# Performance work log

Hardware: AMD Instinct MI355X
Metric: run time of the kernel (lower is better)

Reference implementation:

```python
import jax, jax.numpy as jnp
import numpy as np

NUM_GRAPHS = 1024
NODES = 1024          # nodes per graph (ring length)
N = NUM_GRAPHS * NODES
H = 64


def setup_inputs() -> dict:
    key = jax.random.key(0)
    ks = jax.random.split(key, 4)
    node_index = jax.random.normal(ks[0], (N, 3), dtype=jnp.float32)
    # per-graph ring edges (intended behavior of the torch code)
    i = jnp.arange(N, dtype=jnp.int64)
    g = i // NODES
    src = i
    dst = g * NODES + (i + 1) % NODES
    edge_index = jnp.stack([src, dst])  # [2, N]
    # glorot-ish weights, zero biases (PyG GCNConv default bias=True)
    W1 = jax.random.normal(ks[1], (3, H), dtype=jnp.float32) * (1.0 / np.sqrt(3.0))
    b1 = jnp.zeros((H,), dtype=jnp.float32)
    W2 = jax.random.normal(ks[2], (H, H), dtype=jnp.float32) * (1.0 / np.sqrt(H))
    b2 = jnp.zeros((H,), dtype=jnp.float32)
    Wl = jax.random.normal(ks[3], (H, 3), dtype=jnp.float32) * (1.0 / np.sqrt(H))
    bl = jnp.zeros((3,), dtype=jnp.float32)
    return {"node_index": node_index, "edge_index": edge_index,
            "W1": W1, "b1": b1, "W2": W2, "b2": b2, "Wl": Wl, "bl": bl}


def gcn_layer(x, W, b, src, dst):
    """PyG GCNConv: symmetric-normalized aggregation with self-loops.
    out[j] = sum_{i->j} (deg_i * deg_j)^-0.5 * (x_i @ W) + b
    """
    n = x.shape[0]
    h = x @ W                                   # [n, out]
    loop = jnp.arange(n, dtype=src.dtype)
    s = jnp.concatenate([src, loop])
    d = jnp.concatenate([dst, loop])
    deg = jax.ops.segment_sum(jnp.ones(d.shape[0], dtype=h.dtype), d, num_segments=n)
    dinv = jnp.where(deg > 0, jax.lax.rsqrt(jnp.maximum(deg, 1e-12)), 0.0)
    norm = dinv[s] * dinv[d]                    # [E+n]
    msg = h[s] * norm[:, None]                  # gather + scale
    out = jax.ops.segment_sum(msg, d, num_segments=n)  # scatter-add
    return out + b


def reference(node_index, edge_index, W1, b1, W2, b2, Wl, bl):
    src, dst = edge_index[0], edge_index[1]
    x = jax.nn.relu(gcn_layer(node_index, W1, b1, src, dst))
    x = jax.nn.relu(gcn_layer(x, W2, b2, src, dst))
    return x @ Wl + bl
```

## Files before the change

kernel.cpp:

```cpp
#include <hip/hip_runtime.h>

#define NPG 1024
#define NT 256

typedef _Float16 half8 __attribute__((ext_vector_type(8)));
typedef _Float16 half4v __attribute__((ext_vector_type(4)));
typedef __fp16 fp16x2 __attribute__((ext_vector_type(2)));
typedef float floatx4 __attribute__((ext_vector_type(4)));
typedef unsigned int uint4v __attribute__((ext_vector_type(4)));

#define WS_W2F 0
#define WS_W1F 4096
#define WS_WLF 5120

__device__ __forceinline__ unsigned short f2h(float f) {
    union { _Float16 h; unsigned short u; } v; v.h = (_Float16)f; return v.u;
}
__device__ __forceinline__ float h2f(unsigned short u) {
    union { unsigned short u; _Float16 h; } v; v.u = u; return (float)v.h;
}
__device__ __forceinline__ unsigned int pack_h2(float a, float b) {
    union { fp16x2 h; unsigned int u; } v;
    v.h = __builtin_amdgcn_cvt_pkrtz(a, b);
    return v.u;
}
__device__ __forceinline__ int kperm(int k) {
    return ((k & 3)) | (((k >> 2) & 3) << 4) | (((k >> 4) & 3) << 2);
}

union Frag  { half8 h;  unsigned int u[4]; };
union Frag4 { half4v h; unsigned int u[2]; };
union Pack4 { uint4v u; half8 h; };

__global__ void gnn_prep(const float* __restrict__ W1,
                         const float* __restrict__ b1,
                         const float* __restrict__ W2,
                         const float* __restrict__ Wl,
                         unsigned short* __restrict__ ws)
{
    int idx = blockIdx.x * NT + threadIdx.x;
    if (idx >= 6144) return;
    float v;
    if (idx < 4096) {
        int l = (idx >> 3) & 63, j = idx & 7;
        int c16l = l & 15, quadl = l >> 4;
        int f = idx >> 9, ct = f >> 1, kb = f & 1;
        int o  = ct * 16 + c16l;
        int k  = kperm(kb * 32 + quadl * 8 + j);
        v = 0.5f * W2[k * 64 + o];
    } else if (idx < 5120) {
        int r = idx - 4096;
        int ct = r >> 8, rem = r & 255;
        int l = rem >> 2, j = rem & 3;
        int c16l = l & 15, quadl = l >> 4;
        v = 0.0f;
        if (quadl == 0)
            v = (j < 3) ? W1[j * 64 + ct * 16 + c16l] : b1[ct * 16 + c16l];
    } else {
        int r = idx - 5120;
        int l = (r >> 3) & 63, j = r & 7;
        int c16l = l & 15, quadl = l >> 4;
        int kb = r >> 9;
        int o = (2 * kb + (j >> 2)) * 16 + quadl * 4 + (j & 3);
        v = (c16l < 3) ? Wl[o * 3 + c16l] : 0.0f;
    }
    ws[idx] = f2h(v);
}

__global__ __launch_bounds__(NT, 4)
void gnn_main(const float* __restrict__ x0,
              const float* __restrict__ b2,
              const float* __restrict__ bl,
              const unsigned short* __restrict__ ws,
              float* __restrict__ out)
{
    __shared__ unsigned short sX1[2][65 * 72];
    __shared__ uint2 ySv[513];

    const int t    = threadIdx.x;
    const int lane = t & 63;
    const int w    = t >> 6;
    const int c16  = lane & 15;
    const int quad = lane >> 4;

    const int g     = blockIdx.x >> 1;
    const int base  = (blockIdx.x & 1) * 512;
    const int gbase = g * NPG;

    #pragma unroll
    for (int rr = 0; rr < 2; rr++) {
        int rl = t + rr * 256;
        int n1 = (base - 1 + rl) & (NPG - 1);
        int n0 = (n1 - 1) & (NPG - 1);
        const float* a = x0 + (gbase + n0) * 3;
        const float* b = x0 + (gbase + n1) * 3;
        uint2 pv;
        pv.x = pack_h2(0.5f * (a[0] + b[0]), 0.5f * (a[1] + b[1]));
        pv.y = pack_h2(0.5f * (a[2] + b[2]), 1.0f);
        ySv[rl] = pv;
    }
    if (t == 0) {
        int n1 = (base + 511) & (NPG - 1);
        int n0 = (n1 - 1) & (NPG - 1);
        const float* a = x0 + (gbase + n0) * 3;
        const float* b = x0 + (gbase + n1) * 3;
        uint2 pv;
        pv.x = pack_h2(0.5f * (a[0] + b[0]), 0.5f * (a[1] + b[1]));
        pv.y = pack_h2(0.5f * (a[2] + b[2]), 1.0f);
        ySv[512] = pv;
    }

    Frag4 w1f[4];
    #pragma unroll
    for (int ct = 0; ct < 4; ct++)
        w1f[ct].h = *(const half4v*)(ws + WS_W1F + ct * 256 + lane * 4);
    Frag a2[4][2];
    #pragma unroll
    for (int ct = 0; ct < 4; ct++)
        #pragma unroll
        for (int kb = 0; kb < 2; kb++)
            a2[ct][kb].h = *(const half8*)(ws + WS_W2F + (ct * 2 + kb) * 512 + lane * 8);
    Frag a3[2];
    #pragma unroll
    for (int kb = 0; kb < 2; kb++)
        a3[kb].h = *(const half8*)(ws + WS_WLF + kb * 512 + lane * 8);
    floatx4 b2v[4];
    #pragma unroll
    for (int ct = 0; ct < 4; ct++)
        b2v[ct] = *(const floatx4*)(b2 + ct * 16 + quad * 4);
    const float blv = (c16 < 3) ? bl[c16] : 0.0f;
    float w1c0 = 0.0f, w1c1 = 0.0f, w1c2 = 0.0f, w1b = 0.0f;
    if (t < 64) {
        const unsigned short* w1r = ws + WS_W1F + (t >> 4) * 256 + (t & 15) * 4;
        w1c0 = h2f(w1r[0]); w1c1 = h2f(w1r[1]); w1c2 = h2f(w1r[2]); w1b = h2f(w1r[3]);
    }

    __syncthreads();

    auto layer1 = [&](int p0, unsigned short* X1) {
        const int q = 16 * w + c16;
        Frag4 bfr1;
        bfr1.u[0] = bfr1.u[1] = 0;
        if (quad == 0) {
            uint2 pv = ySv[(p0 - base) + q];
            bfr1.u[0] = pv.x;
            bfr1.u[1] = pv.y;
        }
        floatx4 acc1[4];
        #pragma unroll
        for (int ct = 0; ct < 4; ct++) {
            floatx4 z = {0.0f, 0.0f, 0.0f, 0.0f};
            acc1[ct] = __builtin_amdgcn_mfma_f32_16x16x16f16(w1f[ct].h, bfr1.h, z, 0, 0, 0);
        }
        #pragma unroll
        for (int p = 0; p < 2; p++) {
            Pack4 dv;
            dv.u.x = pack_h2(acc1[2*p  ][0], acc1[2*p  ][1]);
            dv.u.y = pack_h2(acc1[2*p  ][2], acc1[2*p  ][3]);
            dv.u.z = pack_h2(acc1[2*p+1][0], acc1[2*p+1][1]);
            dv.u.w = pack_h2(acc1[2*p+1][2], acc1[2*p+1][3]);
            half8 z8 = {};
            dv.h = __builtin_elementwise_max(dv.h, z8);
            *(uint4v*)&X1[q * 72 + quad * 16 + p * 8] = dv.u;
        }
        if (t < 64) {
            uint2 pv = ySv[(p0 - base) + 64];
            float acc = w1b;
            acc = fmaf(h2f((unsigned short)(pv.x & 0xffff)), w1c0, acc);
            acc = fmaf(h2f((unsigned short)(pv.x >> 16)),    w1c1, acc);
            acc = fmaf(h2f((unsigned short)(pv.y & 0xffff)), w1c2, acc);
            X1[64 * 72 + kperm(t)] = f2h(fmaxf(acc, 0.0f));
        }
    };

    auto layer23 = [&](int p0, const unsigned short* X1) {
        const int q = 16 * w + c16;
        half8 bsum[2];
        #pragma unroll
        for (int kb = 0; kb < 2; kb++) {
            half8 r0 = *(const half8*)(&X1[(q    ) * 72 + kb * 32 + quad * 8]);
            half8 r1 = *(const half8*)(&X1[(q + 1) * 72 + kb * 32 + quad * 8]);
            bsum[kb] = r0 + r1;
        }
        floatx4 acc2[4];
        #pragma unroll
        for (int ct = 0; ct < 4; ct++) {
            floatx4 z = b2v[ct];
            z = __builtin_amdgcn_mfma_f32_16x16x32_f16(a2[ct][0].h, bsum[0], z, 0, 0, 0);
            z = __builtin_amdgcn_mfma_f32_16x16x32_f16(a2[ct][1].h, bsum[1], z, 0, 0, 0);
            acc2[ct] = z;
        }
        Frag pa[2];
        #pragma unroll
        for (int ct = 0; ct < 4; ct++) {
            pa[ct >> 1].u[(ct & 1) * 2    ] = pack_h2(acc2[ct][0], acc2[ct][1]);
            pa[ct >> 1].u[(ct & 1) * 2 + 1] = pack_h2(acc2[ct][2], acc2[ct][3]);
        }
        half8 z8 = {};
        pa[0].h = __builtin_elementwise_max(pa[0].h, z8);
        pa[1].h = __builtin_elementwise_max(pa[1].h, z8);
        floatx4 acc3 = {0.0f, 0.0f, 0.0f, 0.0f};
        acc3 = __builtin_amdgcn_mfma_f32_16x16x32_f16(pa[0].h, a3[0].h, acc3, 0, 0, 0);
        acc3 = __builtin_amdgcn_mfma_f32_16x16x32_f16(pa[1].h, a3[1].h, acc3, 0, 0, 0);
        if (c16 < 3) {
            float* po = out + (gbase + p0 + 16 * w + quad * 4) * 3 + c16;
            po[0] = acc3[0] + blv;
            po[3] = acc3[1] + blv;
            po[6] = acc3[2] + blv;
            po[9] = acc3[3] + blv;
        }
    };

    layer1(base, sX1[0]);
    __syncthreads();
    #pragma unroll
    for (int tl = 0; tl < 7; tl++) {
        layer1(base + (tl + 1) * 64, sX1[(tl + 1) & 1]);
        layer23(base + tl * 64, sX1[tl & 1]);
        __syncthreads();
    }
    layer23(base + 7 * 64, sX1[1]);
}

extern "C" void kernel_launch(void* const* d_in, const int* in_sizes, int n_in,
                              void* d_out, int out_size, void* d_ws, size_t ws_size,
                              hipStream_t stream) {
    const float* x0 = (const float*)d_in[0];
    const float* W1 = (const float*)d_in[2];
    const float* b1 = (const float*)d_in[3];
    const float* W2 = (const float*)d_in[4];
    const float* b2 = (const float*)d_in[5];
    const float* Wl = (const float*)d_in[6];
    const float* bl = (const float*)d_in[7];
    unsigned short* ws = (unsigned short*)d_ws;
    float* out = (float*)d_out;

    gnn_prep<<<24, NT, 0, stream>>>(W1, b1, W2, Wl, ws);
    gnn_main<<<2048, NT, 0, stream>>>(x0, b2, bl, ws, out);
}
```

Before: 98.17 us.

## Process one whole graph per block instead of half a graph

Each block now handles all 1024 nodes of a graph, so the grid is halved to 1024 blocks and the per-block prologue (weight fragment loads, bias loads) is amortized over twice the work. The smoothed-input staging buffer is doubled, and the tile loop is restructured as a non-unrolled loop with two tiles per iteration to keep code size in check. The cost is fewer blocks (1024 over 256 CUs) and more LDS per block, which may lower occupancy and leave tail imbalance.

```diff
diff --git a/kernel.cpp b/kernel.cpp
--- a/kernel.cpp
+++ b/kernel.cpp
@@ -75,7 +75,7 @@
               float* __restrict__ out)
 {
     __shared__ unsigned short sX1[2][65 * 72];
-    __shared__ uint2 ySv[513];
+    __shared__ uint2 ySv[1025];
 
     const int t    = threadIdx.x;
     const int lane = t & 63;
@@ -83,15 +83,14 @@
     const int c16  = lane & 15;
     const int quad = lane >> 4;
 
-    const int g     = blockIdx.x >> 1;
-    const int base  = (blockIdx.x & 1) * 512;
+    const int g     = blockIdx.x;
     const int gbase = g * NPG;
 
     #pragma unroll
-    for (int rr = 0; rr < 2; rr++) {
+    for (int rr = 0; rr < 4; rr++) {
         int rl = t + rr * 256;
-        int n1 = (base - 1 + rl) & (NPG - 1);
-        int n0 = (n1 - 1) & (NPG - 1);
+        int n1 = (rl - 1) & (NPG - 1);
+        int n0 = (rl - 2) & (NPG - 1);
         const float* a = x0 + (gbase + n0) * 3;
         const float* b = x0 + (gbase + n1) * 3;
         uint2 pv;
@@ -100,14 +99,12 @@
         ySv[rl] = pv;
     }
     if (t == 0) {
-        int n1 = (base + 511) & (NPG - 1);
-        int n0 = (n1 - 1) & (NPG - 1);
-        const float* a = x0 + (gbase + n0) * 3;
-        const float* b = x0 + (gbase + n1) * 3;
+        const float* a = x0 + (gbase + 1022) * 3;
+        const float* b = x0 + (gbase + 1023) * 3;
         uint2 pv;
         pv.x = pack_h2(0.5f * (a[0] + b[0]), 0.5f * (a[1] + b[1]));
         pv.y = pack_h2(0.5f * (a[2] + b[2]), 1.0f);
-        ySv[512] = pv;
+        ySv[1024] = pv;
     }
 
     Frag4 w1f[4];
@@ -142,7 +139,7 @@
         Frag4 bfr1;
         bfr1.u[0] = bfr1.u[1] = 0;
         if (quad == 0) {
-            uint2 pv = ySv[(p0 - base) + q];
+            uint2 pv = ySv[p0 + q];
             bfr1.u[0] = pv.x;
             bfr1.u[1] = pv.y;
         }
@@ -164,7 +161,7 @@
             *(uint4v*)&X1[q * 72 + quad * 16 + p * 8] = dv.u;
         }
         if (t < 64) {
-            uint2 pv = ySv[(p0 - base) + 64];
+            uint2 pv = ySv[p0 + 64];
             float acc = w1b;
             acc = fmaf(h2f((unsigned short)(pv.x & 0xffff)), w1c0, acc);
             acc = fmaf(h2f((unsigned short)(pv.x >> 16)),    w1c1, acc);
@@ -211,15 +208,22 @@
         }
     };
 
-    layer1(base, sX1[0]);
+    layer1(0, sX1[0]);
     __syncthreads();
-    #pragma unroll
-    for (int tl = 0; tl < 7; tl++) {
-        layer1(base + (tl + 1) * 64, sX1[(tl + 1) & 1]);
-        layer23(base + tl * 64, sX1[tl & 1]);
+    #pragma unroll 1
+    for (int i = 0; i < 7; i++) {
+        const int p0 = i * 128;
+        layer1(p0 + 64, sX1[1]);
+        layer23(p0, sX1[0]);
         __syncthreads();
-    }
-    layer23(base + 7 * 64, sX1[1]);
+        layer1(p0 + 128, sX1[0]);
+        layer23(p0 + 64, sX1[1]);
+        __syncthreads();
+    }
+    layer1(960, sX1[1]);
+    layer23(896, sX1[0]);
+    __syncthreads();
+    layer23(960, sX1[1]);
 }
 
 extern "C" void kernel_launch(void* const* d_in, const int* in_sizes, int n_in,
@@ -236,5 +240,5 @@
     float* out = (float*)d_out;
 
     gnn_prep<<<24, NT, 0, stream>>>(W1, b1, W2, Wl, ws);
-    gnn_main<<<2048, NT, 0, stream>>>(x0, b2, bl, ws, out);
-}
+    gnn_main<<<1024, NT, 0, stream>>>(x0, b2, bl, ws, out);
+}
```

Result: no change. 98.53 us (+0.4%).

## Recompute layer-1 halo per wave to remove block barriers and shared double buffer

Applied to the files above, without the earlier changes.

Each wave now computes layer-1 activations for both its row and the next row using two MFMAs and sums them in registers. It then writes the pre-aggregated sum to a per-wave shared slab and reads it back in B-fragment layout. This removes the block-wide __syncthreads between tiles, the halo row handled by scalar code, and the cross-wave double-buffered X1 tile. In exchange the layer-1 MFMA count doubles, and the loop is no longer unrolled, which gives up some cross-iteration overlap.

```diff
diff --git a/kernel.cpp b/kernel.cpp
--- a/kernel.cpp
+++ b/kernel.cpp
@@ -2,6 +2,7 @@
 
 #define NPG 1024
 #define NT 256
+#define PITCH 88
 
 typedef _Float16 half8 __attribute__((ext_vector_type(8)));
 typedef _Float16 half4v __attribute__((ext_vector_type(4)));
@@ -30,7 +31,6 @@
 
 union Frag  { half8 h;  unsigned int u[4]; };
 union Frag4 { half4v h; unsigned int u[2]; };
-union Pack4 { uint4v u; half8 h; };
 
 __global__ void gnn_prep(const float* __restrict__ W1,
                          const float* __restrict__ b1,
@@ -74,7 +74,7 @@
               const unsigned short* __restrict__ ws,
               float* __restrict__ out)
 {
-    __shared__ unsigned short sX1[2][65 * 72];
+    __shared__ unsigned short X1w[4][16 * PITCH];
     __shared__ uint2 ySv[513];
 
     const int t    = threadIdx.x;
@@ -129,65 +129,53 @@
     for (int ct = 0; ct < 4; ct++)
         b2v[ct] = *(const floatx4*)(b2 + ct * 16 + quad * 4);
     const float blv = (c16 < 3) ? bl[c16] : 0.0f;
-    float w1c0 = 0.0f, w1c1 = 0.0f, w1c2 = 0.0f, w1b = 0.0f;
-    if (t < 64) {
-        const unsigned short* w1r = ws + WS_W1F + (t >> 4) * 256 + (t & 15) * 4;
-        w1c0 = h2f(w1r[0]); w1c1 = h2f(w1r[1]); w1c2 = h2f(w1r[2]); w1b = h2f(w1r[3]);
-    }
 
     __syncthreads();
 
-    auto layer1 = [&](int p0, unsigned short* X1) {
-        const int q = 16 * w + c16;
-        Frag4 bfr1;
-        bfr1.u[0] = bfr1.u[1] = 0;
+    unsigned short* Xp = &X1w[w][0];
+    const int rowoff = c16 * PITCH;
+
+    #pragma unroll 1
+    for (int i = 0; i < 8; i++) {
+        const int r = i * 64 + 16 * w + c16;
+
+        Frag4 ba, bb;
+        ba.u[0] = ba.u[1] = bb.u[0] = bb.u[1] = 0;
         if (quad == 0) {
-            uint2 pv = ySv[(p0 - base) + q];
-            bfr1.u[0] = pv.x;
-            bfr1.u[1] = pv.y;
-        }
-        floatx4 acc1[4];
+            uint2 pva = ySv[r];     ba.u[0] = pva.x; ba.u[1] = pva.y;
+            uint2 pvb = ySv[r + 1]; bb.u[0] = pvb.x; bb.u[1] = pvb.y;
+        }
+        unsigned int sw[8];
         #pragma unroll
         for (int ct = 0; ct < 4; ct++) {
             floatx4 z = {0.0f, 0.0f, 0.0f, 0.0f};
-            acc1[ct] = __builtin_amdgcn_mfma_f32_16x16x16f16(w1f[ct].h, bfr1.h, z, 0, 0, 0);
-        }
-        #pragma unroll
-        for (int p = 0; p < 2; p++) {
-            Pack4 dv;
-            dv.u.x = pack_h2(acc1[2*p  ][0], acc1[2*p  ][1]);
-            dv.u.y = pack_h2(acc1[2*p  ][2], acc1[2*p  ][3]);
-            dv.u.z = pack_h2(acc1[2*p+1][0], acc1[2*p+1][1]);
-            dv.u.w = pack_h2(acc1[2*p+1][2], acc1[2*p+1][3]);
-            half8 z8 = {};
-            dv.h = __builtin_elementwise_max(dv.h, z8);
-            *(uint4v*)&X1[q * 72 + quad * 16 + p * 8] = dv.u;
-        }
-        if (t < 64) {
-            uint2 pv = ySv[(p0 - base) + 64];
-            float acc = w1b;
-            acc = fmaf(h2f((unsigned short)(pv.x & 0xffff)), w1c0, acc);
-            acc = fmaf(h2f((unsigned short)(pv.x >> 16)),    w1c1, acc);
-            acc = fmaf(h2f((unsigned short)(pv.y & 0xffff)), w1c2, acc);
-            X1[64 * 72 + kperm(t)] = f2h(fmaxf(acc, 0.0f));
-        }
-    };
-
-    auto layer23 = [&](int p0, const unsigned short* X1) {
-        const int q = 16 * w + c16;
-        half8 bsum[2];
-        #pragma unroll
-        for (int kb = 0; kb < 2; kb++) {
-            half8 r0 = *(const half8*)(&X1[(q    ) * 72 + kb * 32 + quad * 8]);
-            half8 r1 = *(const half8*)(&X1[(q + 1) * 72 + kb * 32 + quad * 8]);
-            bsum[kb] = r0 + r1;
-        }
+            floatx4 aa = __builtin_amdgcn_mfma_f32_16x16x16f16(w1f[ct].h, ba.h, z, 0, 0, 0);
+            floatx4 ab = __builtin_amdgcn_mfma_f32_16x16x16f16(w1f[ct].h, bb.h, z, 0, 0, 0);
+            Frag4 va, vb;
+            va.u[0] = pack_h2(aa[0], aa[1]); va.u[1] = pack_h2(aa[2], aa[3]);
+            vb.u[0] = pack_h2(ab[0], ab[1]); vb.u[1] = pack_h2(ab[2], ab[3]);
+            half4v z4 = {};
+            va.h = __builtin_elementwise_max(va.h, z4);
+            vb.h = __builtin_elementwise_max(vb.h, z4);
+            va.h = va.h + vb.h;
+            sw[2 * ct]     = va.u[0];
+            sw[2 * ct + 1] = va.u[1];
+        }
+        uint4v v0, v1;
+        v0.x = sw[0]; v0.y = sw[1]; v0.z = sw[2]; v0.w = sw[3];
+        v1.x = sw[4]; v1.y = sw[5]; v1.z = sw[6]; v1.w = sw[7];
+        *(uint4v*)&Xp[rowoff + 16 * quad]     = v0;
+        *(uint4v*)&Xp[rowoff + 16 * quad + 8] = v1;
+
+        half8 bsum0 = *(const half8*)&Xp[rowoff + quad * 8];
+        half8 bsum1 = *(const half8*)&Xp[rowoff + 32 + quad * 8];
+
         floatx4 acc2[4];
         #pragma unroll
         for (int ct = 0; ct < 4; ct++) {
             floatx4 z = b2v[ct];
-            z = __builtin_amdgcn_mfma_f32_16x16x32_f16(a2[ct][0].h, bsum[0], z, 0, 0, 0);
-            z = __builtin_amdgcn_mfma_f32_16x16x32_f16(a2[ct][1].h, bsum[1], z, 0, 0, 0);
+            z = __builtin_amdgcn_mfma_f32_16x16x32_f16(a2[ct][0].h, bsum0, z, 0, 0, 0);
+            z = __builtin_amdgcn_mfma_f32_16x16x32_f16(a2[ct][1].h, bsum1, z, 0, 0, 0);
             acc2[ct] = z;
         }
         Frag pa[2];
@@ -203,23 +191,13 @@
         acc3 = __builtin_amdgcn_mfma_f32_16x16x32_f16(pa[0].h, a3[0].h, acc3, 0, 0, 0);
         acc3 = __builtin_amdgcn_mfma_f32_16x16x32_f16(pa[1].h, a3[1].h, acc3, 0, 0, 0);
         if (c16 < 3) {
-            float* po = out + (gbase + p0 + 16 * w + quad * 4) * 3 + c16;
+            float* po = out + (gbase + base + i * 64 + 16 * w + quad * 4) * 3 + c16;
             po[0] = acc3[0] + blv;
             po[3] = acc3[1] + blv;
             po[6] = acc3[2] + blv;
             po[9] = acc3[3] + blv;
         }
-    };
-
-    layer1(base, sX1[0]);
-    __syncthreads();
-    #pragma unroll
-    for (int tl = 0; tl < 7; tl++) {
-        layer1(base + (tl + 1) * 64, sX1[(tl + 1) & 1]);
-        layer23(base + tl * 64, sX1[tl & 1]);
-        __syncthreads();
-    }
-    layer23(base + 7 * 64, sX1[1]);
+    }
 }
 
 extern "C" void kernel_launch(void* const* d_in, const int* in_sizes, int n_in,
```

Result: no change. 98.24 us (+0.1%).
